# Optimization experiments

Hardware: AMD Instinct MI355X
Metric: run time of the kernel (lower is better)

Reference implementation:

```python
import jax, jax.numpy as jnp
import numpy as np
from jax import lax

NUM_HEADS = 4
ROPE_BASE = 10000.0


def _rope(x):
    # x: (b, h, w, c). Faithful to the torch RoPE: angles indexed by the h axis
    # with shape (h, c/2), which broadcasts against the w axis (requires h == w).
    b, h, w, c = x.shape
    k_max = c // 2
    theta = 1.0 / (ROPE_BASE ** (jnp.arange(k_max, dtype=x.dtype) / k_max))  # (c/2,)
    angles = jnp.arange(h, dtype=x.dtype)[:, None] * theta  # (h, c/2)
    cos, sin = jnp.cos(angles), jnp.sin(angles)
    xr = x.reshape(b, h, w, k_max, 2)
    re, im = xr[..., 0], xr[..., 1]
    # complex multiply (cos + i sin) * (re + i im); (h, c/2) broadcasts along w
    out_re = cos * re - sin * im
    out_im = sin * re + cos * im
    return jnp.stack([out_re, out_im], axis=-1).reshape(b, h, w, c)


def setup_inputs() -> dict:
    key = jax.random.key(0)
    k1, k2, k3, k4, k5 = jax.random.split(key, 5)
    b, c, h, w = 8, 512, 96, 96
    x = jax.random.normal(k1, (b, c, h, w), dtype=jnp.float32)
    W_qk = jax.random.normal(k2, (2 * c, c), dtype=jnp.float32) * (c ** -0.5)
    b_qk = jax.random.normal(k3, (2 * c,), dtype=jnp.float32) * 0.02
    lepe_w = jax.random.normal(k4, (c, 1, 3, 3), dtype=jnp.float32) * (1.0 / 3.0)
    lepe_b = jax.random.normal(k5, (c,), dtype=jnp.float32) * 0.02
    return {"x": x, "W_qk": W_qk, "b_qk": b_qk, "lepe_w": lepe_w, "lepe_b": lepe_b}


def reference(x, W_qk, b_qk, lepe_w, lepe_b):
    b, c, h, w = x.shape
    n = h * w
    heads = NUM_HEADS
    hd = c // heads

    xs = x.reshape(b, c, n).transpose(0, 2, 1)  # (b, n, c)
    qk = (xs @ W_qk.T + b_qk).reshape(b, n, 2, c)
    q = jax.nn.elu(qk[:, :, 0]) + 1.0  # (b, n, c)
    k = jax.nn.elu(qk[:, :, 1]) + 1.0
    v = xs

    q_rope = _rope(q.reshape(b, h, w, c)).reshape(b, n, heads, hd).transpose(0, 2, 1, 3)
    k_rope = _rope(k.reshape(b, h, w, c)).reshape(b, n, heads, hd).transpose(0, 2, 1, 3)

    # faithful flat reshape (b, n, c) -> (b, heads, n, hd) (splits the n axis)
    q2 = q.reshape(b, heads, n, hd)
    k2 = k.reshape(b, heads, n, hd)
    v2 = v.reshape(b, heads, n, hd)

    k_mean = k2.mean(axis=2, keepdims=True)  # (b, heads, 1, hd)
    z = 1.0 / (jnp.einsum('bhnd,bhmd->bhnm', q2, k_mean) + 1e-6)  # (b, heads, n, 1)

    scale = n ** -0.5
    kv = jnp.einsum('bhnd,bhne->bhde', k_rope * scale, v2 * scale)  # (b, heads, hd, hd)
    out = jnp.einsum('bhnd,bhde->bhne', q_rope, kv) * z  # (b, heads, n, hd)

    out = out.transpose(0, 2, 1, 3).reshape(b, n, c).transpose(0, 2, 1).reshape(b, c, h, w)

    # v2.reshape(b,h,w,c).permute(0,3,1,2) recovers the original (b, c, h, w) layout
    v_img = v2.reshape(b, h, w, c).transpose(0, 3, 1, 2)
    lepe = lax.conv_general_dilated(
        v_img, lepe_w, window_strides=(1, 1), padding='SAME',
        feature_group_count=c, dimension_numbers=('NCHW', 'OIHW', 'NCHW'))
    lepe = lepe + lepe_b[None, :, None, None]
    return out + lepe
```

## Files before the change

### kernel.cpp

```cpp
#include <hip/hip_runtime.h>
#include <hip/hip_bf16.h>
#include <cstdint>

#define BB 8
#define CC 512
#define HH 96
#define NN 9216
#define HEADS 4
#define HD 128
#define KMAX 256

typedef unsigned short ushort_t;
typedef __attribute__((ext_vector_type(8))) short bf16x8;
typedef __attribute__((ext_vector_type(4))) float f32x4;

__device__ __forceinline__ unsigned short f2bf(float f) {
  unsigned int u = __float_as_uint(f);
  u += 0x7fffu + ((u >> 16) & 1u);
  return (unsigned short)(u >> 16);
}
__device__ __forceinline__ float bf2f(unsigned short s) {
  return __uint_as_float(((unsigned int)s) << 16);
}
__device__ __forceinline__ unsigned int pk2(float lo, float hi) {
  return (unsigned int)f2bf(lo) | ((unsigned int)f2bf(hi) << 16);
}

__device__ __forceinline__ void gld16(const void* g, void* l) {
  __builtin_amdgcn_global_load_lds(
      (const __attribute__((address_space(1))) unsigned int*)(uintptr_t)g,
      (__attribute__((address_space(3))) unsigned int*)(unsigned int)(uintptr_t)l,
      16, 0, 0);
}

__global__ void rope_table_k(float* __restrict__ rope) {
  int t = blockIdx.x * 256 + threadIdx.x;
  if (t >= HH * KMAX) return;
  int col = t >> 8;
  int kk = t & (KMAX - 1);
  float theta = powf(10000.0f, -((float)kk) / (float)KMAX);
  float ang = (float)col * theta;
  float s, c;
  sincosf(ang, &s, &c);
  rope[2 * t] = c;
  rope[2 * t + 1] = s;
}

__global__ void conv_w_k(const float* __restrict__ W, unsigned short* __restrict__ Wbf) {
  int t = blockIdx.x * 256 + threadIdx.x;
  float4 v = *(const float4*)(W + (size_t)t * 4);
  unsigned int lo = (unsigned int)f2bf(v.x) | ((unsigned int)f2bf(v.y) << 16);
  unsigned int hi = (unsigned int)f2bf(v.z) | ((unsigned int)f2bf(v.w) << 16);
  *(uint2*)(Wbf + (size_t)t * 4) = make_uint2(lo, hi);
}

__global__ void transpose_xb_k(const float* __restrict__ x, unsigned short* __restrict__ xt,
                               int b) {
  __shared__ unsigned short T[64 * 72];
  const int pos0 = blockIdx.x * 64;
  const int ch0 = blockIdx.y * 64;
  const int tid = threadIdx.x;
#pragma unroll
  for (int i = 0; i < 4; ++i) {
    int fi = i * 256 + tid;
    int ch = fi >> 4, p4 = fi & 15;
    float4 v = *(const float4*)(x + ((size_t)b * CC + ch0 + ch) * NN + pos0 + p4 * 4);
    T[(p4 * 4 + 0) * 72 + ch] = f2bf(v.x);
    T[(p4 * 4 + 1) * 72 + ch] = f2bf(v.y);
    T[(p4 * 4 + 2) * 72 + ch] = f2bf(v.z);
    T[(p4 * 4 + 3) * 72 + ch] = f2bf(v.w);
  }
  __syncthreads();
#pragma unroll
  for (int i = 0; i < 2; ++i) {
    int s = i * 256 + tid;
    int p = s >> 3, cc = s & 7;
    uint4 u = *(const uint4*)&T[p * 72 + cc * 8];
    *(uint4*)(xt + (size_t)(pos0 + p) * CC + ch0 + cc * 8) = u;
  }
}

__launch_bounds__(256)
__global__ void gemm_qk_mfma(const unsigned short* __restrict__ xt,
                             const unsigned short* __restrict__ Wbf,
                             const float* __restrict__ bqk,
                             unsigned short* __restrict__ qout,
                             unsigned short* __restrict__ kout, int b) {
  __shared__ __align__(16) unsigned short sA[128 * 64];
  __shared__ __align__(16) unsigned short sB[128 * 64];
  const int tid = threadIdx.x;
  const int wv = tid >> 6, lane = tid & 63;
  const int bn = blockIdx.x;
  const int m0 = blockIdx.y * 128;
  const int j0 = bn * 128;
  const int row = lane & 15, quad = lane >> 4;
  const int mt0 = (wv & 1) * 64, nt0 = (wv >> 1) * 64;
  f32x4 acc[4][4];
#pragma unroll
  for (int mi = 0; mi < 4; ++mi)
#pragma unroll
    for (int ni = 0; ni < 4; ++ni) acc[mi][ni] = (f32x4){0.f, 0.f, 0.f, 0.f};

  for (int kt = 0; kt < CC; kt += 64) {
#pragma unroll
    for (int it = 0; it < 4; ++it) {
      int s = it * 256 + tid;
      int srow = s >> 3;
      int sc = (s & 7) ^ (srow & 7);
      int ldsoff = (it * 256 + wv * 64) * 8;
      gld16(xt + (size_t)(m0 + srow) * CC + kt + sc * 8, &sA[ldsoff]);
      gld16(Wbf + (size_t)(j0 + srow) * CC + kt + sc * 8, &sB[ldsoff]);
    }
    __syncthreads();
#pragma unroll
    for (int ks = 0; ks < 2; ++ks) {
      bf16x8 af[4], bf[4];
      const int chunk = (ks * 4 + quad) ^ (row & 7);
#pragma unroll
      for (int mi = 0; mi < 4; ++mi)
        af[mi] = *(const bf16x8*)&sA[((mt0 + mi * 16 + row) * 8 + chunk) * 8];
#pragma unroll
      for (int ni = 0; ni < 4; ++ni)
        bf[ni] = *(const bf16x8*)&sB[((nt0 + ni * 16 + row) * 8 + chunk) * 8];
#pragma unroll
      for (int mi = 0; mi < 4; ++mi)
#pragma unroll
        for (int ni = 0; ni < 4; ++ni)
          acc[mi][ni] = __builtin_amdgcn_mfma_f32_16x16x32_bf16(af[mi], bf[ni], acc[mi][ni], 0, 0, 0);
    }
    __syncthreads();
  }
  unsigned short* dst = (j0 < CC) ? qout : kout;
  const int jl = (j0 & (CC - 1)) + nt0;
  float bj[4];
#pragma unroll
  for (int ni = 0; ni < 4; ++ni) bj[ni] = bqk[j0 + nt0 + ni * 16 + row];
#pragma unroll
  for (int mi = 0; mi < 4; ++mi) {
#pragma unroll
    for (int ni = 0; ni < 4; ++ni) {
#pragma unroll
      for (int r = 0; r < 4; ++r) {
        float v = acc[mi][ni][r] + bj[ni];
        v = v > 0.f ? v + 1.f : expm1f(v) + 1.f;
        int mrow = m0 + mt0 + mi * 16 + quad * 4 + r;
        dst[((size_t)b * NN + mrow) * CC + jl + ni * 16 + row] = f2bf(v);
      }
    }
  }
}

__global__ void kmean_p1_k(const unsigned short* __restrict__ kbf, float* __restrict__ part) {
  __shared__ float red[256];
  const int seg = blockIdx.x;
  const int bh = blockIdx.y;
  const int b = bh >> 2, head = bh & 3;
  const int tid = threadIdx.x;
  const int d = tid & 127, half = tid >> 7;
  const unsigned short* base =
      kbf + ((size_t)b * NN + head * 2304 + seg * 128 + half * 64) * CC + d;
  float sum = 0.f;
  for (int pp = 0; pp < 64; ++pp) {
    const unsigned short* rp = base + (size_t)pp * CC;
    sum += bf2f(rp[0]) + bf2f(rp[128]) + bf2f(rp[256]) + bf2f(rp[384]);
  }
  red[tid] = sum;
  __syncthreads();
  if (half == 0) part[((size_t)bh * 18 + seg) * 128 + d] = red[d] + red[d + 128];
}

__global__ void kmean_p2_k(const float* __restrict__ part, float* __restrict__ kmean) {
  int idx = blockIdx.x * 256 + threadIdx.x;
  int bh = idx >> 7, d = idx & 127;
  float s = 0.f;
#pragma unroll
  for (int i = 0; i < 18; ++i) s += part[((size_t)bh * 18 + i) * 128 + d];
  kmean[idx] = s * (1.0f / 9216.0f);
}

__global__ void z_k(const unsigned short* __restrict__ qbf, const float* __restrict__ kmean,
                    float* __restrict__ z) {
  const int wv = threadIdx.x >> 6, lane = threadIdx.x & 63;
  const int zbase = (blockIdx.x * 4 + wv) * 8;
  const int bh = zbase / NN;
  const int p0 = zbase % NN;
  const int b = bh >> 2, head = bh & 3;
  const float km0 = kmean[bh * 128 + lane * 2];
  const float km1 = kmean[bh * 128 + lane * 2 + 1];
#pragma unroll
  for (int it = 0; it < 8; ++it) {
    const int p = p0 + it;
    const int pos = head * 2304 + (p >> 2);
    const int chb = (p & 3) * 128;
    const unsigned short* qp = qbf + ((size_t)b * NN + pos) * CC + chb + lane * 2;
    float dot = bf2f(qp[0]) * km0 + bf2f(qp[1]) * km1;
#pragma unroll
    for (int off = 1; off < 64; off <<= 1) dot += __shfl_xor(dot, off, 64);
    if (lane == 0) z[zbase + it] = 1.0f / (dot + 1e-6f);
  }
}

__launch_bounds__(256, 2)
__global__ void kv_mfma_k(const unsigned short* __restrict__ kbf, const float* __restrict__ x,
                          const float* __restrict__ rope, float* __restrict__ kvp) {
  __shared__ __align__(16) unsigned short sK[128 * 64];
  const int s = blockIdx.x;
  const int bh = blockIdx.y;
  const int b = bh >> 2, head = bh & 3;
  const int tid = threadIdx.x;
  const int wv = tid >> 6, lane = tid & 63;
  const int row = lane & 15, quad = lane >> 4;
  const int e0 = (wv & 1) * 64, d0 = (wv >> 1) * 64;
  const int r = s >> 2;
  const int t0 = (s & 3) * 576;

  const int qg = tid & 7;
  const int dg = (tid >> 3) * 4;
  const unsigned short* kbase = kbf + (size_t)b * NN * CC + head * HD + dg;
  const int pairb = head * 64 + (dg >> 1);

  f32x4 acc[4][4];
#pragma unroll
  for (int mi = 0; mi < 4; ++mi)
#pragma unroll
    for (int ni = 0; ni < 4; ++ni) acc[mi][ni] = (f32x4){0.f, 0.f, 0.f, 0.f};

  for (int ck = 0; ck < 9; ++ck) {
    const int tc = t0 + ck * 64;
    float4 a0[8], a1[8];
#pragma unroll
    for (int mi = 0; mi < 4; ++mi)
#pragma unroll
      for (int ks = 0; ks < 2; ++ks) {
        const float* xp = x + (size_t)(b * CC + r * 128 + e0 + mi * 16 + row) * NN +
                          head * 2304 + tc + ks * 32 + quad * 8;
        a0[mi * 2 + ks] = *(const float4*)xp;
        a1[mi * 2 + ks] = *(const float4*)(xp + 4);
      }
    {
      int p = 4 * (tc + qg * 8) + r;
      int col = p % 96;
      float rw0[8], rw1[8], rw2[8], rw3[8];
#pragma unroll
      for (int j = 0; j < 8; ++j) {
        uint2 kv2 = *(const uint2*)(kbase + (size_t)p * CC);
        const float* rp = rope + ((size_t)col * KMAX + pairb) * 2;
        float4 cs = *(const float4*)rp;
        float re0 = bf2f((unsigned short)(kv2.x & 0xffffu));
        float im0 = bf2f((unsigned short)(kv2.x >> 16));
        float re1 = bf2f((unsigned short)(kv2.y & 0xffffu));
        float im1 = bf2f((unsigned short)(kv2.y >> 16));
        rw0[j] = cs.x * re0 - cs.y * im0;
        rw1[j] = cs.y * re0 + cs.x * im0;
        rw2[j] = cs.z * re1 - cs.w * im1;
        rw3[j] = cs.w * re1 + cs.z * im1;
        p += 4;
        col += 4;
        col = (col >= 96) ? col - 96 : col;
      }
#pragma unroll
      for (int rr = 0; rr < 4; ++rr) {
        const float* rw = (rr == 0) ? rw0 : (rr == 1) ? rw1 : (rr == 2) ? rw2 : rw3;
        const int d = dg + rr;
        uint4 pk;
        pk.x = pk2(rw[0], rw[1]);
        pk.y = pk2(rw[2], rw[3]);
        pk.z = pk2(rw[4], rw[5]);
        pk.w = pk2(rw[6], rw[7]);
        *(uint4*)&sK[(d * 8 + (qg ^ (d & 7))) * 8] = pk;
      }
    }
    __syncthreads();
#pragma unroll
    for (int ks = 0; ks < 2; ++ks) {
      bf16x8 bfr[4];
#pragma unroll
      for (int ni = 0; ni < 4; ++ni) {
        const int d = d0 + ni * 16 + row;
        const int o = (ks * 4 + quad) ^ (d & 7);
        bfr[ni] = *(const bf16x8*)&sK[(d * 8 + o) * 8];
      }
#pragma unroll
      for (int mi = 0; mi < 4; ++mi) {
        const int f = mi * 2 + ks;
        union { bf16x8 v; unsigned int u[4]; } af;
        af.u[0] = pk2(a0[f].x, a0[f].y);
        af.u[1] = pk2(a0[f].z, a0[f].w);
        af.u[2] = pk2(a1[f].x, a1[f].y);
        af.u[3] = pk2(a1[f].z, a1[f].w);
#pragma unroll
        for (int ni = 0; ni < 4; ++ni)
          acc[mi][ni] = __builtin_amdgcn_mfma_f32_16x16x32_bf16(af.v, bfr[ni], acc[mi][ni], 0, 0, 0);
      }
    }
    __syncthreads();
  }
  float* dst = kvp + (size_t)(s * 32 + bh) * (HD * HD);
#pragma unroll
  for (int mi = 0; mi < 4; ++mi) {
#pragma unroll
    for (int ni = 0; ni < 4; ++ni) {
#pragma unroll
      for (int rr = 0; rr < 4; ++rr) {
        const int e = e0 + mi * 16 + quad * 4 + rr;
        const int d = d0 + ni * 16 + row;
        dst[e * HD + d] = acc[mi][ni][rr];
      }
    }
  }
}

__global__ void kv_reduce_k(const float* __restrict__ kvp, unsigned short* __restrict__ kvtb) {
  int idx = blockIdx.x * 256 + threadIdx.x;
  float ssum = 0.f;
#pragma unroll
  for (int i = 0; i < 16; ++i) ssum += kvp[(size_t)i * (32 * HD * HD) + idx];
  kvtb[idx] = f2bf(ssum * (1.0f / 9216.0f));
}

__launch_bounds__(256)
__global__ void out_mfma_k(const unsigned short* __restrict__ qbf,
                           const unsigned short* __restrict__ kvtb,
                           const float* __restrict__ z, const float* __restrict__ rope,
                           float* __restrict__ out) {
  const int bh = blockIdx.y, b = bh >> 2, head = bh & 3;
  const int pos0 = blockIdx.x * 128;
  const int tid = threadIdx.x, wv = tid >> 6, lane = tid & 63;
  const int row = lane & 15, quad = lane >> 4;
  const int e0 = (wv & 1) * 64;
  const int p0 = (wv >> 1) * 64;
  f32x4 acc[4][4];
#pragma unroll
  for (int mi = 0; mi < 4; ++mi)
#pragma unroll
    for (int ni = 0; ni < 4; ++ni) acc[mi][ni] = (f32x4){0.f, 0.f, 0.f, 0.f};

  int posn[4], coln[4];
#pragma unroll
  for (int ni = 0; ni < 4; ++ni) {
    posn[ni] = pos0 + p0 + ni * 16 + row;
    coln[ni] = posn[ni] % 96;
  }

#pragma unroll
  for (int kt = 0; kt < HD; kt += 32) {
    bf16x8 af[4], bfr[4];
#pragma unroll
    for (int mi = 0; mi < 4; ++mi)
      af[mi] = *(const bf16x8*)&kvtb[((size_t)bh * HD + e0 + mi * 16 + row) * HD + kt + quad * 8];
#pragma unroll
    for (int ni = 0; ni < 4; ++ni) {
      const uint4 u = *(const uint4*)(qbf + ((size_t)b * NN + posn[ni]) * CC +
                                      head * HD + kt + quad * 8);
      const int pairb = head * 64 + (kt >> 1) + quad * 4;
      const float* rp = rope + ((size_t)coln[ni] * KMAX + pairb) * 2;
      float4 r0 = *(const float4*)rp;
      float4 r1 = *(const float4*)(rp + 4);
      unsigned int uu[4] = {u.x, u.y, u.z, u.w};
      float cs[8] = {r0.x, r0.y, r0.z, r0.w, r1.x, r1.y, r1.z, r1.w};
      bf16x8 bb;
#pragma unroll
      for (int pr = 0; pr < 4; ++pr) {
        float re = bf2f((unsigned short)(uu[pr] & 0xffffu));
        float im = bf2f((unsigned short)(uu[pr] >> 16));
        float c = cs[2 * pr], s = cs[2 * pr + 1];
        bb[2 * pr] = (short)f2bf(c * re - s * im);
        bb[2 * pr + 1] = (short)f2bf(s * re + c * im);
      }
      bfr[ni] = bb;
    }
#pragma unroll
    for (int mi = 0; mi < 4; ++mi)
#pragma unroll
      for (int ni = 0; ni < 4; ++ni)
        acc[mi][ni] = __builtin_amdgcn_mfma_f32_16x16x32_bf16(af[mi], bfr[ni], acc[mi][ni], 0, 0, 0);
  }
  float zv[4];
#pragma unroll
  for (int ni = 0; ni < 4; ++ni) zv[ni] = z[(size_t)bh * NN + posn[ni]];
#pragma unroll
  for (int mi = 0; mi < 4; ++mi) {
#pragma unroll
    for (int ni = 0; ni < 4; ++ni) {
#pragma unroll
      for (int r = 0; r < 4; ++r) {
        int e = e0 + mi * 16 + quad * 4 + r;
        out[((size_t)b * CC + head * HD + e) * NN + posn[ni]] = acc[mi][ni][r] * zv[ni];
      }
    }
  }
}

__global__ void lepe_k(const float* __restrict__ x, const float* __restrict__ lw,
                       const float* __restrict__ lb, float* __restrict__ out) {
  const int blk = blockIdx.x;
  const int bc = blk / 9;
  const int tile = blk - bc * 9;
  const int ch = bc & (CC - 1);
  const float* wp = lw + ch * 9;
  float w[9];
#pragma unroll
  for (int t = 0; t < 9; ++t) w[t] = wp[t];
  const float bias = lb[ch];
  const float* xp = x + (size_t)bc * NN;
  const int pos = tile * 1024 + threadIdx.x * 4;
  const int pi = pos / 96;
  const int pj = pos - pi * 96;

  float4 o = *(const float4*)(out + (size_t)bc * NN + pos);

  float a0 = bias, a1 = bias, a2 = bias, a3 = bias;
#pragma unroll
  for (int r = 0; r < 3; ++r) {
    const int y = pi + r - 1;
    if ((unsigned)y >= 96u) continue;
    const float* rowp = xp + y * 96 + pj;
    float4 M = *(const float4*)rowp;
    float Lv = (pj > 0) ? rowp[-1] : 0.f;
    float Rv = (pj < 92) ? rowp[4] : 0.f;
    const float w0 = w[r * 3 + 0], w1 = w[r * 3 + 1], w2 = w[r * 3 + 2];
    a0 += w0 * Lv + w1 * M.x + w2 * M.y;
    a1 += w0 * M.x + w1 * M.y + w2 * M.z;
    a2 += w0 * M.y + w1 * M.z + w2 * M.w;
    a3 += w0 * M.z + w1 * M.w + w2 * Rv;
  }
  o.x += a0; o.y += a1; o.z += a2; o.w += a3;
  *(float4*)(out + (size_t)bc * NN + pos) = o;
}

extern "C" void kernel_launch(void* const* d_in, const int* in_sizes, int n_in,
                              void* d_out, int out_size, void* d_ws, size_t ws_size,
                              hipStream_t stream) {
  const float* x = (const float*)d_in[0];
  const float* Wqk = (const float*)d_in[1];
  const float* bqk = (const float*)d_in[2];
  const float* lw = (const float*)d_in[3];
  const float* lb = (const float*)d_in[4];
  float* out = (float*)d_out;
  char* ws = (char*)d_ws;
  unsigned short* qbf = (unsigned short*)(ws);
  unsigned short* kbf = (unsigned short*)(ws + 75497472);
  float* rope = (float*)(ws + 150994944);
  float* kmean = (float*)(ws + 151191552);
  float* z = (float*)(ws + 151207936);
  float* kvp = (float*)(ws + 152387584);
  unsigned short* xtb = (unsigned short*)(ws + 152387584);
  float* kmean_part = (float*)(ws + 152387584 + 16777216);
  unsigned short* kvtb = (unsigned short*)(ws + 185942016);
  unsigned short* Wbf = (unsigned short*)(ws + 188039168);

  conv_w_k<<<dim3(512), dim3(256), 0, stream>>>(Wqk, Wbf);
  rope_table_k<<<dim3(96), dim3(256), 0, stream>>>(rope);
  for (int b = 0; b < BB; ++b) {
    transpose_xb_k<<<dim3(144, 8), dim3(256), 0, stream>>>(x, xtb, b);
    gemm_qk_mfma<<<dim3(8, 72), dim3(256), 0, stream>>>(xtb, Wbf, bqk, qbf, kbf, b);
  }
  kmean_p1_k<<<dim3(18, 32), dim3(256), 0, stream>>>(kbf, kmean_part);
  kmean_p2_k<<<dim3(16), dim3(256), 0, stream>>>(kmean_part, kmean);
  z_k<<<dim3(9216), dim3(256), 0, stream>>>(qbf, kmean, z);
  kv_mfma_k<<<dim3(16, 32), dim3(256), 0, stream>>>(kbf, x, rope, kvp);
  kv_reduce_k<<<dim3(2048), dim3(256), 0, stream>>>(kvp, kvtb);
  out_mfma_k<<<dim3(72, 32), dim3(256), 0, stream>>>(qbf, kvtb, z, rope, out);
  lepe_k<<<dim3(36864), dim3(256), 0, stream>>>(x, lw, lb, out);
}
```

Before: 871.1 us.

## Fuse LePE depthwise conv into attention output kernel via LDS transpose

```diff
diff --git a/kernel.cpp b/kernel.cpp
--- a/kernel.cpp
+++ b/kernel.cpp
@@ -319,10 +319,12 @@
 }
 
 __launch_bounds__(256)
-__global__ void out_mfma_k(const unsigned short* __restrict__ qbf,
+__global__ void out_lepe_k(const unsigned short* __restrict__ qbf,
                            const unsigned short* __restrict__ kvtb,
                            const float* __restrict__ z, const float* __restrict__ rope,
-                           float* __restrict__ out) {
+                           const float* __restrict__ x, const float* __restrict__ lw,
+                           const float* __restrict__ lb, float* __restrict__ out) {
+  __shared__ __align__(16) float Ts[64 * 132];
   const int bh = blockIdx.y, b = bh >> 2, head = bh & 3;
   const int pos0 = blockIdx.x * 128;
   const int tid = threadIdx.x, wv = tid >> 6, lane = tid & 63;
@@ -375,57 +377,69 @@
       for (int ni = 0; ni < 4; ++ni)
         acc[mi][ni] = __builtin_amdgcn_mfma_f32_16x16x32_bf16(af[mi], bfr[ni], acc[mi][ni], 0, 0, 0);
   }
-  float zv[4];
-#pragma unroll
-  for (int ni = 0; ni < 4; ++ni) zv[ni] = z[(size_t)bh * NN + posn[ni]];
-#pragma unroll
-  for (int mi = 0; mi < 4; ++mi) {
-#pragma unroll
-    for (int ni = 0; ni < 4; ++ni) {
-#pragma unroll
-      for (int r = 0; r < 4; ++r) {
-        int e = e0 + mi * 16 + quad * 4 + r;
-        out[((size_t)b * CC + head * HD + e) * NN + posn[ni]] = acc[mi][ni][r] * zv[ni];
-      }
-    }
-  }
-}
-
-__global__ void lepe_k(const float* __restrict__ x, const float* __restrict__ lw,
-                       const float* __restrict__ lb, float* __restrict__ out) {
-  const int blk = blockIdx.x;
-  const int bc = blk / 9;
-  const int tile = blk - bc * 9;
-  const int ch = bc & (CC - 1);
-  const float* wp = lw + ch * 9;
-  float w[9];
-#pragma unroll
-  for (int t = 0; t < 9; ++t) w[t] = wp[t];
-  const float bias = lb[ch];
-  const float* xp = x + (size_t)bc * NN;
-  const int pos = tile * 1024 + threadIdx.x * 4;
-  const int pi = pos / 96;
-  const int pj = pos - pi * 96;
-
-  float4 o = *(const float4*)(out + (size_t)bc * NN + pos);
-
-  float a0 = bias, a1 = bias, a2 = bias, a3 = bias;
-#pragma unroll
-  for (int r = 0; r < 3; ++r) {
-    const int y = pi + r - 1;
-    if ((unsigned)y >= 96u) continue;
-    const float* rowp = xp + y * 96 + pj;
-    float4 M = *(const float4*)rowp;
-    float Lv = (pj > 0) ? rowp[-1] : 0.f;
-    float Rv = (pj < 92) ? rowp[4] : 0.f;
-    const float w0 = w[r * 3 + 0], w1 = w[r * 3 + 1], w2 = w[r * 3 + 2];
-    a0 += w0 * Lv + w1 * M.x + w2 * M.y;
-    a1 += w0 * M.x + w1 * M.y + w2 * M.z;
-    a2 += w0 * M.y + w1 * M.z + w2 * M.w;
-    a3 += w0 * M.z + w1 * M.w + w2 * Rv;
-  }
-  o.x += a0; o.y += a1; o.z += a2; o.w += a3;
-  *(float4*)(out + (size_t)bc * NN + pos) = o;
+#pragma unroll
+  for (int ni = 0; ni < 4; ++ni) {
+    const float zn = z[(size_t)bh * NN + posn[ni]];
+#pragma unroll
+    for (int mi = 0; mi < 4; ++mi)
+#pragma unroll
+      for (int r = 0; r < 4; ++r) acc[mi][ni][r] *= zn;
+  }
+
+  const int t5 = tid >> 5, tl = tid & 31;
+#pragma unroll
+  for (int h = 0; h < 2; ++h) {
+    if ((wv & 1) == h) {
+#pragma unroll
+      for (int mi = 0; mi < 4; ++mi)
+#pragma unroll
+        for (int ni = 0; ni < 4; ++ni)
+#pragma unroll
+          for (int r = 0; r < 4; ++r) {
+            const int eL = mi * 16 + quad * 4 + r;
+            const int p = p0 + ni * 16 + row;
+            Ts[eL * 132 + p] = acc[mi][ni][r];
+          }
+    }
+    __syncthreads();
+#pragma unroll 2
+    for (int i = 0; i < 8; ++i) {
+      const int eL = i * 8 + t5;
+      const int ch = head * HD + h * 64 + eL;
+      const int pos = pos0 + tl * 4;
+      const int pi = pos / 96;
+      const int pj = pos - pi * 96;
+      const float* wp = lw + ch * 9;
+      float w[9];
+#pragma unroll
+      for (int t = 0; t < 9; ++t) w[t] = wp[t];
+      const float* xp = x + ((size_t)b * CC + ch) * NN;
+      const float bias = lb[ch];
+      float a0 = bias, a1 = bias, a2 = bias, a3 = bias;
+#pragma unroll
+      for (int rr = 0; rr < 3; ++rr) {
+        const int y = pi + rr - 1;
+        if ((unsigned)y >= 96u) continue;
+        const float* rowp = xp + y * 96 + pj;
+        float4 M = *(const float4*)rowp;
+        float Lv = (pj > 0) ? rowp[-1] : 0.f;
+        float Rv = (pj < 92) ? rowp[4] : 0.f;
+        const float w0 = w[rr * 3 + 0], w1 = w[rr * 3 + 1], w2 = w[rr * 3 + 2];
+        a0 += w0 * Lv + w1 * M.x + w2 * M.y;
+        a1 += w0 * M.x + w1 * M.y + w2 * M.z;
+        a2 += w0 * M.y + w1 * M.z + w2 * M.w;
+        a3 += w0 * M.z + w1 * M.w + w2 * Rv;
+      }
+      const float4 attn = *(const float4*)&Ts[eL * 132 + tl * 4];
+      float4 o;
+      o.x = attn.x + a0;
+      o.y = attn.y + a1;
+      o.z = attn.z + a2;
+      o.w = attn.w + a3;
+      *(float4*)(out + ((size_t)b * CC + ch) * NN + pos) = o;
+    }
+    __syncthreads();
+  }
 }
 
 extern "C" void kernel_launch(void* const* d_in, const int* in_sizes, int n_in,
@@ -460,6 +474,5 @@
   z_k<<<dim3(9216), dim3(256), 0, stream>>>(qbf, kmean, z);
   kv_mfma_k<<<dim3(16, 32), dim3(256), 0, stream>>>(kbf, x, rope, kvp);
   kv_reduce_k<<<dim3(2048), dim3(256), 0, stream>>>(kvp, kvtb);
-  out_mfma_k<<<dim3(72, 32), dim3(256), 0, stream>>>(qbf, kvtb, z, rope, out);
-  lepe_k<<<dim3(36864), dim3(256), 0, stream>>>(x, lw, lb, out);
-}
+  out_lepe_k<<<dim3(72, 32), dim3(256), 0, stream>>>(qbf, kvtb, z, rope, x, lw, lb, out);
+}
```

Measured after the change: 926.4 us. 1.06x slower.
